# Optimization experiments

Hardware: AMD Instinct MI355X
Metric: run time of the kernel (lower is better)

## Reference

```python
import jax, jax.numpy as jnp
import numpy as np

KS, AS = 13, 12  # kernel_size (12 vertices + center), anchor_size (icosahedron vertices)


def _icosa():
    # Icosahedron oriented with vertex 0 on +z (required by sort_level_vs xy-rotation logic)
    r5 = np.sqrt(5.0); rr = 2.0 / r5
    vs = [[0.0, 0.0, 1.0]]
    for k in range(5):
        t = 2.0 * np.pi * k / 5.0
        vs.append([rr * np.cos(t), rr * np.sin(t), 1.0 / r5])
    for k in range(5):
        t = 2.0 * np.pi * k / 5.0 + np.pi / 5.0
        vs.append([rr * np.cos(t), rr * np.sin(t), -1.0 / r5])
    vs.append([0.0, 0.0, -1.0])
    return np.array(vs)


def _rotm(axis, ang):
    a = np.asarray(axis, dtype=np.float64); a = a / np.linalg.norm(a)
    K = np.array([[0, -a[2], a[1]], [a[2], 0, -a[0]], [-a[1], a[0], 0]])
    return np.eye(3) + np.sin(ang) * K + (1.0 - np.cos(ang)) * (K @ K)


def _ico_group(vs):
    # Generate the 60-element icosahedral rotation group by closure from two generators
    gens = [_rotm([0.0, 0.0, 1.0], 2 * np.pi / 5), _rotm(vs[1], 2 * np.pi / 5)]
    group = [np.eye(3)]
    keys = {tuple(np.round(np.eye(3), 4).ravel())}
    frontier = [np.eye(3)]
    while frontier:
        nxt = []
        for g in frontier:
            for h in gens:
                c = h @ g
                k = tuple(np.round(c, 4).ravel())
                if k not in keys:
                    keys.add(k); group.append(c); nxt.append(c)
        frontier = nxt
    return group


def _sort_level_vs(v_idxs, vs):
    # Faithful port of sort_level_vs: order ring vertices by successive 72-deg xy rotations
    out = [v_idxs[0]]
    vs_l = vs[v_idxs][:, :2]
    cur = vs_l[[0]]
    dth = 2 * np.pi / 5
    R = np.array([[np.cos(dth), -np.sin(dth)], [np.sin(dth), np.cos(dth)]])
    for _ in range(4):
        cur = R.dot(cur.T).T
        out.append(v_idxs[np.argmin(np.abs(vs_l - cur).sum(1))])
    return np.array(out)


def _build_buffers():
    vs = _icosa()
    dots = vs @ vs.T
    v0_adjs = np.where(np.abs(dots[0] - 1.0 / np.sqrt(5)) < 1e-6)[0]
    v0_lv2 = np.where(np.abs(dots[0] + 1.0 / np.sqrt(5)) < 1e-6)[0]
    v0_opp = int(np.argmin(dots[0]))
    # 12 rotation anchors: one group element mapping vertex 0 to each vertex
    group = _ico_group(vs)
    vRs = []
    for i in range(12):
        for R in group:
            if np.linalg.norm(R @ vs[0] - vs[i]) < 1e-5:
                vRs.append(R); break
    vRs = np.stack(vRs)  # [12,3,3]
    rot_v = np.einsum('rij,aj->rai', vRs, vs)  # [12,12,3]
    d = np.linalg.norm(rot_v[:, :, None, :] - vs[None, None], axis=-1)
    trace_idx_ori = np.argmin(d, axis=2)  # [12,12] vertex permutation per anchor rotation
    trace_idx_rot = np.empty_like(trace_idx_ori)
    for r in range(12):
        trace_idx_rot[r, trace_idx_ori[r]] = np.arange(12)
    trace_idxv_rot = np.concatenate([trace_idx_rot, np.full((12, 1), 12, np.int64)], axis=1)  # [12,13]
    # idx_map: faithful port of the __init__ construction (maps 13*12 slots -> 36 weight params)
    inv = np.empty(12, np.int64)
    inv[0] = 0; inv[v0_adjs] = 1; inv[v0_lv2] = 2; inv[v0_opp] = 3
    a_s = _sort_level_vs(v0_adjs, vs)
    l_s = _sort_level_vs(v0_lv2, vs)
    idx_map = np.empty(KS * AS, np.int64)
    idx_map[:AS] = inv
    idx_map[v0_opp * AS:(v0_opp + 1) * AS] = inv + 4
    idx_map[-AS:] = inv + 8
    seq1 = np.arange(12, 24); seq2 = np.arange(24, 36)
    idx_map[a_s[0] * AS:(a_s[0] + 1) * AS] = seq1
    idx_map[l_s[0] * AS:(l_s[0] + 1) * AS] = seq2
    shifts = [[4, 0, 1, 2, 3], [3, 4, 0, 1, 2], [2, 3, 4, 0, 1], [1, 2, 3, 4, 0]]
    for j, sh in enumerate(shifts, start=1):
        new = np.empty(12, np.int64)
        new[a_s] = a_s[sh]; new[l_s] = l_s[sh]
        new[0] = 0; new[v0_opp] = v0_opp
        idx_map[a_s[j] * AS:(a_s[j] + 1) * AS] = seq1[new]
        idx_map[l_s[j] * AS:(l_s[j] + 1) * AS] = seq2[new]
    return idx_map, trace_idxv_rot, trace_idx_rot


def setup_inputs() -> dict:
    key = jax.random.key(0)
    k1, k2 = jax.random.split(key)
    B, CIN, COUT, P = 8, 16, 16, 4096
    x = jax.random.normal(k1, (B, CIN, KS, P, AS), dtype=jnp.float32)
    W = jax.random.normal(k2, (COUT, CIN, 36), dtype=jnp.float32) * 0.05  # xavier-scale
    idx_map, tivr, tir = _build_buffers()
    return {
        'x': x,
        'W': W,
        'idx_map': jnp.asarray(idx_map, jnp.int32),
        'trace_idxv_rot': jnp.asarray(tivr, jnp.int32),
        'trace_idx_rot': jnp.asarray(tir, jnp.int32),
    }


def reference(x, W, idx_map, trace_idxv_rot, trace_idx_rot):
    d_out, d_in, _ = W.shape
    # Expand 36 free params to the [d, c, k, a] kernel via idx_map gather
    Wm = W[:, :, idx_map].reshape(d_out, d_in, KS, AS)
    # The two torch.gather calls (dims 2 then 3) collapse to:
    # Wfull[d,c,k,a,r] = Wm[d,c, trace_idxv_rot[r,k], trace_idx_rot[r,a]]
    Wfull = Wm[:, :, trace_idxv_rot[:, :, None], trace_idx_rot[:, None, :]]  # [d,c,r,k,a]
    return jnp.einsum('dcrka,bckpa->bdpr', Wfull, x)
```

## Files before the change

### kernel.cpp

```cpp
#include <hip/hip_runtime.h>

#define B_    8
#define CIN_  16
#define COUT_ 16
#define KS_   13
#define AS_   12
#define P_    4096
#define R_    12
#define M_    192
#define KTOT  2496
#define BN    128
#define KT    96
#define NSTEP 26
#define LDP   104

typedef float  f32x4  __attribute__((ext_vector_type(4)));
typedef __bf16 bf16x4 __attribute__((ext_vector_type(4)));
typedef __bf16 bf16x8 __attribute__((ext_vector_type(8)));

__global__ void build_wmat(const float* __restrict__ W,
                           const int* __restrict__ idx_map,
                           const int* __restrict__ tivr,
                           const int* __restrict__ tir,
                           __bf16* __restrict__ Wmat) {
  int m = blockIdx.x;
  int d = m / R_;
  int r = m - d * R_;
  for (int kap = threadIdx.x; kap < KTOT; kap += blockDim.x) {
    int c = kap / (KS_ * AS_);
    int t = kap - c * (KS_ * AS_);
    int k = t / AS_;
    int a = t - k * AS_;
    int s = idx_map[tivr[r * KS_ + k] * AS_ + tir[r * AS_ + a]];
    Wmat[m * KTOT + kap] = (__bf16)W[(d * CIN_ + c) * 36 + s];
  }
}

__global__ __launch_bounds__(512, 2)
void s2conv(const float* __restrict__ x,
            const __bf16* __restrict__ Wmat,
            float* __restrict__ out) {
  __shared__ __bf16 Ws[2][M_][LDP];
  __shared__ __bf16 Xs[2][BN][LDP];

  const int tid  = threadIdx.x;
  const int lane = tid & 63;
  const int wave = tid >> 6;
  const int wm   = wave >> 2;
  const int wn   = wave & 3;
  const int l15  = lane & 15;
  const int l4   = lane >> 4;

  const int wg = blockIdx.x;
  const int b  = wg >> 5;
  const int p0 = (wg & 31) << 7;

  int wrow[4], wchk[4];
#pragma unroll
  for (int j = 0; j < 4; ++j) {
    int i = tid + j * 512;
    wrow[j] = i / 12;
    wchk[j] = i - wrow[j] * 12;
  }
  const int ti   = 2048 + (tid >> 1);
  const int trow = ti / 12;
  const int tchk = ti - trow * 12;
  const int thalf = (tid & 1) * 8;

  f32x4 acc[6][2];
#pragma unroll
  for (int i = 0; i < 6; ++i)
#pragma unroll
    for (int j = 0; j < 2; ++j)
      acc[i][j] = f32x4{0.f, 0.f, 0.f, 0.f};

  auto load_x = [&](int kt, f32x4 (&st)[6]) {
    int ck = kt * 8 + wave;
    const f32x4* bp =
        (const f32x4*)(x + (size_t)(b * 208 + ck) * 49152 + (size_t)p0 * 12);
#pragma unroll
    for (int it = 0; it < 6; ++it) st[it] = bp[it * 64 + lane];
  };

  auto load_w = [&](int kt, bf16x8 (&w4)[4], bf16x4& wt) {
    const char* wb = (const char*)Wmat + (size_t)kt * (KT * 2);
#pragma unroll
    for (int j = 0; j < 4; ++j)
      w4[j] = *(const bf16x8*)(wb + (size_t)wrow[j] * (KTOT * 2) + wchk[j] * 16);
    wt = *(const bf16x4*)(wb + (size_t)trow * (KTOT * 2) + tchk * 16 + thalf);
  };

  auto write_tiles = [&](int buf, f32x4 (&st)[6], bf16x8 (&w4)[4], bf16x4& wt) {
    char* wsb = (char*)&Ws[buf][0][0];
    char* xsb = (char*)&Xs[buf][0][0];
#pragma unroll
    for (int j = 0; j < 4; ++j)
      *(bf16x8*)(wsb + wrow[j] * (LDP * 2) + wchk[j] * 16) = w4[j];
    *(bf16x4*)(wsb + trow * (LDP * 2) + tchk * 16 + thalf) = wt;
#pragma unroll
    for (int it = 0; it < 6; ++it) {
      int f4i = it * 64 + lane;
      int pl  = f4i / 3;
      int a   = (f4i - pl * 3) * 4;
      bf16x4 v = __builtin_convertvector(st[it], bf16x4);
      *(bf16x4*)(xsb + pl * (LDP * 2) + (wave * 12 + a) * 2) = v;
    }
  };

  auto mfma_step = [&](int buf) {
    const __bf16* wsb = &Ws[buf][0][0];
    const __bf16* xsb = &Xs[buf][0][0];
#pragma unroll
    for (int ks = 0; ks < 3; ++ks) {
      const int col = ks * 32 + l4 * 8;
      bf16x8 af[6], bfr[2];
#pragma unroll
      for (int mt = 0; mt < 6; ++mt)
        af[mt] = *(const bf16x8*)(wsb + (wm * 96 + mt * 16 + l15) * LDP + col);
#pragma unroll
      for (int nt = 0; nt < 2; ++nt)
        bfr[nt] = *(const bf16x8*)(xsb + (wn * 32 + nt * 16 + l15) * LDP + col);
#pragma unroll
      for (int mt = 0; mt < 6; ++mt)
#pragma unroll
        for (int nt = 0; nt < 2; ++nt)
          acc[mt][nt] = __builtin_amdgcn_mfma_f32_16x16x32_bf16(
              af[mt], bfr[nt], acc[mt][nt], 0, 0, 0);
    }
  };

  auto barrier = [&]() {
    asm volatile("s_waitcnt lgkmcnt(0)" ::: "memory");
    __builtin_amdgcn_s_barrier();
  };

  f32x4  stA[6], stB[6];
  bf16x8 wA4[4], wB4[4];
  bf16x4 wAt, wBt;
  load_x(0, stA); load_w(0, wA4, wAt);
  load_x(1, stB); load_w(1, wB4, wBt);
  write_tiles(0, stA, wA4, wAt);
  barrier();

  for (int kt = 0; kt < NSTEP - 2; kt += 2) {
    load_x(kt + 2, stA); load_w(kt + 2, wA4, wAt);
    __builtin_amdgcn_sched_barrier(0);
    write_tiles(1, stB, wB4, wBt);
    mfma_step(0);
    barrier();

    load_x(kt + 3, stB); load_w(kt + 3, wB4, wBt);
    __builtin_amdgcn_sched_barrier(0);
    write_tiles(0, stA, wA4, wAt);
    mfma_step(1);
    barrier();
  }

  write_tiles(1, stB, wB4, wBt);
  mfma_step(0);
  barrier();
  mfma_step(1);

#pragma unroll
  for (int mt = 0; mt < 6; ++mt) {
    int mrow0 = wm * 96 + mt * 16 + l4 * 4;
    int d  = mrow0 / 12;
    int r0 = mrow0 - d * 12;
#pragma unroll
    for (int nt = 0; nt < 2; ++nt) {
      int p = p0 + wn * 32 + nt * 16 + l15;
      float* dst = out + (size_t)((b * 16 + d) * 4096 + p) * 12 + r0;
      *(f32x4*)dst = acc[mt][nt];
    }
  }
}

extern "C" void kernel_launch(void* const* d_in, const int* in_sizes, int n_in,
                              void* d_out, int out_size, void* d_ws, size_t ws_size,
                              hipStream_t stream) {
  const float* x       = (const float*)d_in[0];
  const float* W       = (const float*)d_in[1];
  const int*   idx_map = (const int*)d_in[2];
  const int*   tivr    = (const int*)d_in[3];
  const int*   tir     = (const int*)d_in[4];
  float*       out     = (float*)d_out;
  __bf16*      Wmat    = (__bf16*)d_ws;

  build_wmat<<<dim3(M_), dim3(256), 0, stream>>>(W, idx_map, tivr, tir, Wmat);
  s2conv<<<dim3(256), dim3(512), 0, stream>>>(x, Wmat, out);
}
```

Measured before the change: 78.08 us.

## Pre-swizzle weights into MFMA fragment layout and load them directly to registers

The weight-expansion kernel now writes the bf16 weight matrix in per-lane MFMA A-fragment order, so the main kernel can load each wave's 18 A fragments per k-step with coalesced global loads straight into registers. The shared-memory weight tile and its writes and reads are removed, which cuts LDS traffic and footprint. In exchange each wave issues more global loads per step, and these are not prefetched a step ahead, so their latency may be exposed and register pressure rises.

```diff
diff --git a/kernel.cpp b/kernel.cpp
--- a/kernel.cpp
+++ b/kernel.cpp
@@ -18,29 +18,41 @@
 typedef __bf16 bf16x4 __attribute__((ext_vector_type(4)));
 typedef __bf16 bf16x8 __attribute__((ext_vector_type(8)));
 
-__global__ void build_wmat(const float* __restrict__ W,
-                           const int* __restrict__ idx_map,
-                           const int* __restrict__ tivr,
-                           const int* __restrict__ tir,
-                           __bf16* __restrict__ Wmat) {
-  int m = blockIdx.x;
-  int d = m / R_;
-  int r = m - d * R_;
-  for (int kap = threadIdx.x; kap < KTOT; kap += blockDim.x) {
+__global__ void build_wmatf(const float* __restrict__ W,
+                            const int* __restrict__ idx_map,
+                            const int* __restrict__ tivr,
+                            const int* __restrict__ tir,
+                            __bf16* __restrict__ WmatF) {
+  int gid  = blockIdx.x * blockDim.x + threadIdx.x;
+  int lane = gid & 63;
+  int fid  = gid >> 6;
+  int kt   = fid / 36;
+  int rem  = fid - kt * 36;
+  int mt   = rem / 3;
+  int ks   = rem - mt * 3;
+
+  int row = mt * 16 + (lane & 15);
+  int d = row / R_;
+  int r = row - d * R_;
+
+  bf16x8 v;
+#pragma unroll
+  for (int e = 0; e < 8; ++e) {
+    int kap = kt * KT + ks * 32 + (lane >> 4) * 8 + e;
     int c = kap / (KS_ * AS_);
     int t = kap - c * (KS_ * AS_);
     int k = t / AS_;
     int a = t - k * AS_;
     int s = idx_map[tivr[r * KS_ + k] * AS_ + tir[r * AS_ + a]];
-    Wmat[m * KTOT + kap] = (__bf16)W[(d * CIN_ + c) * 36 + s];
+    v[e] = (__bf16)W[(d * CIN_ + c) * 36 + s];
   }
+  *(bf16x8*)(WmatF + (size_t)gid * 8) = v;
 }
 
 __global__ __launch_bounds__(512, 2)
 void s2conv(const float* __restrict__ x,
-            const __bf16* __restrict__ Wmat,
+            const __bf16* __restrict__ WmatF,
             float* __restrict__ out) {
-  __shared__ __bf16 Ws[2][M_][LDP];
   __shared__ __bf16 Xs[2][BN][LDP];
 
   const int tid  = threadIdx.x;
@@ -54,18 +66,6 @@
   const int wg = blockIdx.x;
   const int b  = wg >> 5;
   const int p0 = (wg & 31) << 7;
-
-  int wrow[4], wchk[4];
-#pragma unroll
-  for (int j = 0; j < 4; ++j) {
-    int i = tid + j * 512;
-    wrow[j] = i / 12;
-    wchk[j] = i - wrow[j] * 12;
-  }
-  const int ti   = 2048 + (tid >> 1);
-  const int trow = ti / 12;
-  const int tchk = ti - trow * 12;
-  const int thalf = (tid & 1) * 8;
 
   f32x4 acc[6][2];
 #pragma unroll
@@ -82,21 +82,16 @@
     for (int it = 0; it < 6; ++it) st[it] = bp[it * 64 + lane];
   };
 
-  auto load_w = [&](int kt, bf16x8 (&w4)[4], bf16x4& wt) {
-    const char* wb = (const char*)Wmat + (size_t)kt * (KT * 2);
+  auto load_a = [&](int kt, bf16x8 (&af)[18]) {
+    const char* base = (const char*)WmatF +
+        (size_t)(kt * 36 + wm * 18) * 1024 + lane * 16;
 #pragma unroll
-    for (int j = 0; j < 4; ++j)
-      w4[j] = *(const bf16x8*)(wb + (size_t)wrow[j] * (KTOT * 2) + wchk[j] * 16);
-    wt = *(const bf16x4*)(wb + (size_t)trow * (KTOT * 2) + tchk * 16 + thalf);
+    for (int f = 0; f < 18; ++f)
+      af[f] = *(const bf16x8*)(base + f * 1024);
   };
 
-  auto write_tiles = [&](int buf, f32x4 (&st)[6], bf16x8 (&w4)[4], bf16x4& wt) {
-    char* wsb = (char*)&Ws[buf][0][0];
+  auto write_X = [&](int buf, f32x4 (&st)[6]) {
     char* xsb = (char*)&Xs[buf][0][0];
-#pragma unroll
-    for (int j = 0; j < 4; ++j)
-      *(bf16x8*)(wsb + wrow[j] * (LDP * 2) + wchk[j] * 16) = w4[j];
-    *(bf16x4*)(wsb + trow * (LDP * 2) + tchk * 16 + thalf) = wt;
 #pragma unroll
     for (int it = 0; it < 6; ++it) {
       int f4i = it * 64 + lane;
@@ -107,16 +102,12 @@
     }
   };
 
-  auto mfma_step = [&](int buf) {
-    const __bf16* wsb = &Ws[buf][0][0];
+  auto mfma_step = [&](int buf, bf16x8 (&af)[18]) {
     const __bf16* xsb = &Xs[buf][0][0];
 #pragma unroll
     for (int ks = 0; ks < 3; ++ks) {
       const int col = ks * 32 + l4 * 8;
-      bf16x8 af[6], bfr[2];
-#pragma unroll
-      for (int mt = 0; mt < 6; ++mt)
-        af[mt] = *(const bf16x8*)(wsb + (wm * 96 + mt * 16 + l15) * LDP + col);
+      bf16x8 bfr[2];
 #pragma unroll
       for (int nt = 0; nt < 2; ++nt)
         bfr[nt] = *(const bf16x8*)(xsb + (wn * 32 + nt * 16 + l15) * LDP + col);
@@ -125,7 +116,7 @@
 #pragma unroll
         for (int nt = 0; nt < 2; ++nt)
           acc[mt][nt] = __builtin_amdgcn_mfma_f32_16x16x32_bf16(
-              af[mt], bfr[nt], acc[mt][nt], 0, 0, 0);
+              af[mt * 3 + ks], bfr[nt], acc[mt][nt], 0, 0, 0);
     }
   };
 
@@ -135,31 +126,34 @@
   };
 
   f32x4  stA[6], stB[6];
-  bf16x8 wA4[4], wB4[4];
-  bf16x4 wAt, wBt;
-  load_x(0, stA); load_w(0, wA4, wAt);
-  load_x(1, stB); load_w(1, wB4, wBt);
-  write_tiles(0, stA, wA4, wAt);
+  bf16x8 af[18];
+  load_x(0, stA);
+  load_x(1, stB);
+  write_X(0, stA);
   barrier();
 
   for (int kt = 0; kt < NSTEP - 2; kt += 2) {
-    load_x(kt + 2, stA); load_w(kt + 2, wA4, wAt);
+    load_a(kt, af);
+    load_x(kt + 2, stA);
     __builtin_amdgcn_sched_barrier(0);
-    write_tiles(1, stB, wB4, wBt);
-    mfma_step(0);
+    write_X(1, stB);
+    mfma_step(0, af);
     barrier();
 
-    load_x(kt + 3, stB); load_w(kt + 3, wB4, wBt);
+    load_a(kt + 1, af);
+    load_x(kt + 3, stB);
     __builtin_amdgcn_sched_barrier(0);
-    write_tiles(0, stA, wA4, wAt);
-    mfma_step(1);
+    write_X(0, stA);
+    mfma_step(1, af);
     barrier();
   }
 
-  write_tiles(1, stB, wB4, wBt);
-  mfma_step(0);
+  load_a(24, af);
+  write_X(1, stB);
+  mfma_step(0, af);
   barrier();
-  mfma_step(1);
+  load_a(25, af);
+  mfma_step(1, af);
 
 #pragma unroll
   for (int mt = 0; mt < 6; ++mt) {
@@ -184,8 +178,8 @@
   const int*   tivr    = (const int*)d_in[3];
   const int*   tir     = (const int*)d_in[4];
   float*       out     = (float*)d_out;
-  __bf16*      Wmat    = (__bf16*)d_ws;
+  __bf16*      WmatF   = (__bf16*)d_ws;
 
-  build_wmat<<<dim3(M_), dim3(256), 0, stream>>>(W, idx_map, tivr, tir, Wmat);
-  s2conv<<<dim3(256), dim3(512), 0, stream>>>(x, Wmat, out);
+  build_wmatf<<<dim3(117), dim3(512), 0, stream>>>(W, idx_map, tivr, tir, WmatF);
+  s2conv<<<dim3(256), dim3(512), 0, stream>>>(x, WmatF, out);
 }
```

After: 82.35 us. 5.5% more time.
